# Kernel optimization log

Hardware: AMD Instinct MI355X
Metric: run time of the kernel (lower is better)

Reference implementation:

```python
import jax, jax.numpy as jnp
import numpy as np

NUM_HEADS = 4
NUM_GROUPS = 8
EPS = 1e-5


def setup_inputs() -> dict:
    key = jax.random.key(0)
    ks = jax.random.split(key, 4)
    B, C, H, W = 4, 256, 64, 64
    x = jax.random.normal(ks[0], (B, C, H, W), dtype=jnp.float32)
    gn_w = jnp.ones((C,), dtype=jnp.float32)
    gn_b = jnp.zeros((C,), dtype=jnp.float32)
    # 1x1 convs == per-pixel matmuls; store kernels as [out_ch, in_ch]
    w_qkv = jax.random.normal(ks[1], (3 * C, C), dtype=jnp.float32) * (1.0 / np.sqrt(C))
    b_qkv = jnp.zeros((3 * C,), dtype=jnp.float32)
    w_proj = jax.random.normal(ks[2], (C, C), dtype=jnp.float32) * (1.0 / np.sqrt(C))
    b_proj = jnp.zeros((C,), dtype=jnp.float32)
    return {"x": x, "gn_w": gn_w, "gn_b": gn_b, "w_qkv": w_qkv,
            "b_qkv": b_qkv, "w_proj": w_proj, "b_proj": b_proj}


def reference(x, gn_w, gn_b, w_qkv, b_qkv, w_proj, b_proj):
    B, C, H, W = x.shape
    N = H * W
    nh = NUM_HEADS
    dh = C // nh

    # GroupNorm(8, C)
    xg = x.reshape(B, NUM_GROUPS, C // NUM_GROUPS, N)
    mu = jnp.mean(xg, axis=(2, 3), keepdims=True)
    var = jnp.var(xg, axis=(2, 3), keepdims=True)
    h = ((xg - mu) * jax.lax.rsqrt(var + EPS)).reshape(B, C, N)
    h = h * gn_w[None, :, None] + gn_b[None, :, None]

    # qkv 1x1 conv
    qkv = jnp.einsum('oc,bcn->bon', w_qkv, h) + b_qkv[None, :, None]
    q, k, v = jnp.split(qkv, 3, axis=1)  # each [B, C, N]
    q = q.reshape(B, nh, dh, N)
    k = k.reshape(B, nh, dh, N)
    v = v.reshape(B, nh, dh, N)

    # attn = softmax(q^T k / sqrt(dh)) over last dim -> [B, nh, N, N]
    scores = jnp.einsum('bhdi,bhdj->bhij', q, k) / jnp.sqrt(jnp.array(dh, dtype=x.dtype))
    attn = jax.nn.softmax(scores, axis=-1)

    # out = attn @ v^T, back to channel-major layout
    out = jnp.einsum('bhij,bhdj->bhdi', attn, v).reshape(B, C, N)

    # proj_out 1x1 conv + residual
    out = jnp.einsum('oc,bcn->bon', w_proj, out) + b_proj[None, :, None]
    return x + out.reshape(B, C, H, W)
```

## Files before the change

kernel.cpp:

```cpp
#include <hip/hip_runtime.h>
#include <math.h>

#define N_PIX 4096
#define C_CH  256
#define NH    4
#define DH    64

typedef __attribute__((ext_vector_type(8))) short bf16x8;
typedef __attribute__((ext_vector_type(4))) float f32x4;

static __device__ __forceinline__ unsigned short f2bf(float f) {
  union { float f; unsigned u; } v; v.f = f;
  unsigned r = v.u + 0x7fffu + ((v.u >> 16) & 1u);
  return (unsigned short)(r >> 16);
}
static __device__ __forceinline__ unsigned pk2(float a, float b) {
  return (unsigned)f2bf(a) | ((unsigned)f2bf(b) << 16);
}
static __device__ __forceinline__ unsigned pk2t(float a, float b) {
  return __builtin_amdgcn_perm(__float_as_uint(b), __float_as_uint(a),
                               0x07060302u);
}
#if __has_builtin(__builtin_amdgcn_exp2f)
#define EXP2(x) __builtin_amdgcn_exp2f(x)
#else
#define EXP2(x) exp2f(x)
#endif
static __device__ __forceinline__ int swz(int row, int g) {
  return (row << 6) + ((((row >> 2) ^ row ^ g) & 7) << 3);
}

__global__ __launch_bounds__(256) void gn_part_kernel(
    const float* __restrict__ x, const float* __restrict__ wqkv,
    const float* __restrict__ wproj, float* __restrict__ part,
    unsigned short* __restrict__ wB) {
  const int g = blockIdx.x, b = blockIdx.y, z = blockIdx.z;
  const int t = threadIdx.x;
  {
    const int bid = blockIdx.z * 32 + blockIdx.y * 8 + blockIdx.x;
    const int i = bid * 256 + t;
    const float* src = (i < 49152) ? (wqkv + (size_t)i * 4)
                                   : (wproj + (size_t)(i - 49152) * 4);
    float4 v = *(const float4*)src;
    uint2 u;
    u.x = pk2(v.x, v.y);
    u.y = pk2(v.z, v.w);
    *(uint2*)(wB + (size_t)i * 4) = u;
  }
  const float* base = x + (size_t)(b * C_CH + g * 32 + z * 4) * N_PIX;
  float sum = 0.f, sq = 0.f;
  for (int i = t * 4; i < 4 * N_PIX; i += 256 * 4) {
    float4 v = *(const float4*)(base + i);
    sum += v.x + v.y + v.z + v.w;
    sq  += v.x * v.x + v.y * v.y + v.z * v.z + v.w * v.w;
  }
  for (int off = 32; off >= 1; off >>= 1) {
    sum += __shfl_down(sum, off, 64);
    sq  += __shfl_down(sq,  off, 64);
  }
  __shared__ float ps[4], pq[4];
  if ((t & 63) == 0) { ps[t >> 6] = sum; pq[t >> 6] = sq; }
  __syncthreads();
  if (t == 0) {
    int idx = ((b * 8 + g) * 8 + z) * 2;
    part[idx + 0] = ps[0] + ps[1] + ps[2] + ps[3];
    part[idx + 1] = pq[0] + pq[1] + pq[2] + pq[3];
  }
}

__global__ __launch_bounds__(256) void gn_apply_kernel(
    const float* __restrict__ x, const float* __restrict__ part,
    const float* __restrict__ gn_w, const float* __restrict__ gn_b,
    unsigned short* __restrict__ hT) {
  const int n0 = blockIdx.x * 64;
  const int c0 = blockIdx.y * 64;
  const int b  = blockIdx.z;
  const int t  = threadIdx.x;
  __shared__ unsigned short Ht[64 * 64];
  __shared__ float ls[64], lsh[64];
  if (t < 64) {
    int c = c0 + t;
    int g = c >> 5;
    float S = 0.f, Q = 0.f;
#pragma unroll
    for (int z = 0; z < 8; ++z) {
      int idx = ((b * 8 + g) * 8 + z) * 2;
      S += part[idx + 0];
      Q += part[idx + 1];
    }
    const float inv_cnt = 1.f / (32.f * N_PIX);
    float mu  = S * inv_cnt;
    float var = Q * inv_cnt - mu * mu;
    float rstd = rsqrtf(var + 1e-5f);
    float s = rstd * gn_w[c];
    ls[t]  = s;
    lsh[t] = gn_b[c] - mu * s;
  }
  __syncthreads();
  const int cl = t >> 4;
  const int nl = (t & 15) * 4;
#pragma unroll
  for (int r = 0; r < 4; ++r) {
    int ce = cl + r * 16;
    float sv = ls[ce], sh = lsh[ce];
    float4 v =
        *(const float4*)(x + ((size_t)(b * C_CH + c0 + ce)) * N_PIX + n0 + nl);
#pragma unroll
    for (int i = 0; i < 4; ++i) {
      float f = ((const float*)&v)[i] * sv + sh;
      Ht[swz(nl + i, ce >> 3) + (ce & 7)] = f2bf(f);
    }
  }
  __syncthreads();
  {
    const int row = t >> 2, sg = (t & 3) * 2;
    uint4 o0 = *(const uint4*)&Ht[swz(row, sg + 0)];
    uint4 o1 = *(const uint4*)&Ht[swz(row, sg + 1)];
    size_t go = ((size_t)(b * N_PIX + n0 + row)) * C_CH + c0 + sg * 8;
    *(uint4*)(hT + go) = o0;
    *(uint4*)(hT + go + 8) = o1;
  }
}

__global__ __launch_bounds__(256) void qkv_gemm_kernel(
    const unsigned short* __restrict__ hT, const unsigned short* __restrict__ wB,
    const float* __restrict__ bqkv, unsigned short* __restrict__ qT,
    unsigned short* __restrict__ kT, unsigned short* __restrict__ vO) {
  const int head = blockIdx.x;
  const int n0 = blockIdx.y * 128;
  const int b  = blockIdx.z;
  const int t  = threadIdx.x;
  const int wave = t >> 6, lane = t & 63, quad = lane >> 4, lc = lane & 15;

  __shared__ unsigned short Ws[3 * 64 * 64];
  __shared__ unsigned short Hs[128 * 64];

  f32x4 acc[3][4][2];
#pragma unroll
  for (int ty = 0; ty < 3; ++ty)
#pragma unroll
    for (int i = 0; i < 4; ++i)
#pragma unroll
      for (int j = 0; j < 2; ++j) acc[ty][i][j] = (f32x4){0.f, 0.f, 0.f, 0.f};

  const int wrow = t >> 2, wgb = (t & 3) * 2;
  const int hrow = t >> 1, hgb = (t & 1) * 4;
  const unsigned short* wp =
      wB + (size_t)(head * 64 + wrow) * C_CH + wgb * 8;
  const unsigned short* ap =
      hT + ((size_t)(b * N_PIX + n0 + hrow)) * C_CH + hgb * 8;
  const int wsw0 = swz(wrow, wgb + 0), wsw1 = swz(wrow, wgb + 1);
  int hsw[4];
#pragma unroll
  for (int j = 0; j < 4; ++j) hsw[j] = swz(hrow, hgb + j);

  for (int kc = 0; kc < 4; ++kc) {
    const int k0 = kc * 64;
    __syncthreads();
#pragma unroll
    for (int ty = 0; ty < 3; ++ty) {
      const unsigned short* s0 = wp + (size_t)ty * 256 * C_CH + k0;
      uint4 u0 = *(const uint4*)(s0);
      uint4 u1 = *(const uint4*)(s0 + 8);
      *(uint4*)&Ws[ty * 4096 + wsw0] = u0;
      *(uint4*)&Ws[ty * 4096 + wsw1] = u1;
    }
    {
      const unsigned short* s0 = ap + k0;
#pragma unroll
      for (int j = 0; j < 4; ++j) {
        uint4 u = *(const uint4*)(s0 + j * 8);
        *(uint4*)&Hs[hsw[j]] = u;
      }
    }
    __syncthreads();
#pragma unroll
    for (int kh = 0; kh < 2; ++kh) {
      bf16x8 hf[2];
#pragma unroll
      for (int nt = 0; nt < 2; ++nt)
        hf[nt] = *(const bf16x8*)&Hs[swz(wave * 32 + nt * 16 + lc, kh * 4 + quad)];
#pragma unroll
      for (int ty = 0; ty < 3; ++ty) {
        bf16x8 wf[4];
#pragma unroll
        for (int mt = 0; mt < 4; ++mt)
          wf[mt] =
              *(const bf16x8*)&Ws[ty * 4096 + swz(mt * 16 + lc, kh * 4 + quad)];
        if (ty < 2) {
#pragma unroll
          for (int mt = 0; mt < 4; ++mt)
#pragma unroll
            for (int nt = 0; nt < 2; ++nt)
              acc[ty][mt][nt] = __builtin_amdgcn_mfma_f32_16x16x32_bf16(
                  wf[mt], hf[nt], acc[ty][mt][nt], 0, 0, 0);
        } else {
#pragma unroll
          for (int mt = 0; mt < 4; ++mt)
#pragma unroll
            for (int nt = 0; nt < 2; ++nt)
              acc[2][mt][nt] = __builtin_amdgcn_mfma_f32_16x16x32_bf16(
                  hf[nt], wf[mt], acc[2][mt][nt], 0, 0, 0);
        }
      }
    }
  }

#pragma unroll
  for (int ty = 0; ty < 2; ++ty) {
    unsigned short* dst = (ty == 0) ? qT : kT;
    const float qs = (ty == 0) ? 0.125f * 1.44269504f : 1.0f;
    const int bb = ty * 256 + head * 64;
#pragma unroll
    for (int mt = 0; mt < 4; ++mt)
#pragma unroll
      for (int nt = 0; nt < 2; ++nt) {
        int n = n0 + wave * 32 + nt * 16 + lc;
        int d0 = mt * 16 + quad * 4;
        float b0 = bqkv[bb + d0 + 0], b1 = bqkv[bb + d0 + 1];
        float b2 = bqkv[bb + d0 + 2], b3 = bqkv[bb + d0 + 3];
        uint2 w;
        w.x = pk2((acc[ty][mt][nt][0] + b0) * qs, (acc[ty][mt][nt][1] + b1) * qs);
        w.y = pk2((acc[ty][mt][nt][2] + b2) * qs, (acc[ty][mt][nt][3] + b3) * qs);
        *(uint2*)(dst + ((size_t)((b * NH + head) * N_PIX + n)) * 64 + d0) = w;
      }
  }
  {
    const int bb = 512 + head * 64;
#pragma unroll
    for (int mt = 0; mt < 4; ++mt)
#pragma unroll
      for (int nt = 0; nt < 2; ++nt) {
        int d = mt * 16 + lc;
        float bias = bqkv[bb + d];
        int pix = n0 + wave * 32 + nt * 16 + quad * 4;
        uint2 w;
        w.x = pk2(acc[2][mt][nt][0] + bias, acc[2][mt][nt][1] + bias);
        w.y = pk2(acc[2][mt][nt][2] + bias, acc[2][mt][nt][3] + bias);
        *(uint2*)(vO + ((size_t)((b * NH + head) * 64 + d)) * N_PIX + pix) = w;
      }
  }
}

__global__ __launch_bounds__(256) void attn_kernel(
    const unsigned short* __restrict__ qT, const unsigned short* __restrict__ kT,
    const unsigned short* __restrict__ vO, unsigned short* __restrict__ aT) {
  const int t  = threadIdx.x;
  const int i0 = blockIdx.x * 128;
  const int h  = blockIdx.y;
  const int b  = blockIdx.z;
  const size_t bh = (size_t)(b * NH + h);
  const unsigned short* qp = qT + bh * N_PIX * 64;
  const unsigned short* kp = kT + bh * N_PIX * 64;
  const unsigned short* vp = vO + bh * 64 * N_PIX;

  __shared__ unsigned short Qt[128 * 64];
  __shared__ unsigned short Kt[2 * 64 * 64];
  __shared__ unsigned short Vs[2 * 64 * 64];
  unsigned short* const Ps = Qt;

  const int wave = t >> 6, lane = t & 63, quad = lane >> 4, lc = lane & 15;
  const int qb0 = wave * 32, qb1 = wave * 32 + 16;
  const int srow = t >> 2, sg = (t & 3) * 2;
  const int qrow = t >> 1, qg = (t & 1) * 4;

  {
    const unsigned short* sp = qp + (size_t)(i0 + qrow) * 64 + qg * 8;
#pragma unroll
    for (int i = 0; i < 4; ++i) {
      uint4 u = *(const uint4*)(sp + i * 8);
      *(uint4*)&Qt[swz(qrow, qg + i)] = u;
    }
  }
  __syncthreads();
  bf16x8 aq[2][2];
  aq[0][0] = *(const bf16x8*)&Qt[swz(qb0 + lc, quad)];
  aq[0][1] = *(const bf16x8*)&Qt[swz(qb0 + lc, quad + 4)];
  aq[1][0] = *(const bf16x8*)&Qt[swz(qb1 + lc, quad)];
  aq[1][1] = *(const bf16x8*)&Qt[swz(qb1 + lc, quad + 4)];

  int kof0[4], kof1[4], vof0[4], vof1[4], pw[2][4];
#pragma unroll
  for (int jt = 0; jt < 4; ++jt) {
    kof0[jt] = swz(jt * 16 + lc, quad);
    kof1[jt] = swz(jt * 16 + lc, quad + 4);
    pw[0][jt] = swz(qb0 + lc, jt * 2 + (quad >> 1)) + (quad & 1) * 4;
    pw[1][jt] = swz(qb1 + lc, jt * 2 + (quad >> 1)) + (quad & 1) * 4;
  }
#pragma unroll
  for (int mt = 0; mt < 4; ++mt) {
    vof0[mt] = swz(mt * 16 + lc, quad);
    vof1[mt] = swz(mt * 16 + lc, quad + 4);
  }
  const int pb00 = swz(qb0 + lc, quad), pb01 = swz(qb0 + lc, quad + 4);
  const int pb10 = swz(qb1 + lc, quad), pb11 = swz(qb1 + lc, quad + 4);
  const int sw0 = swz(srow, sg + 0), sw1 = swz(srow, sg + 1);
  const unsigned short* kbase = kp + (size_t)srow * 64 + sg * 8;
  const unsigned short* vbase = vp + (size_t)srow * N_PIX + sg * 8;

  float la0 = 0.f, la1 = 0.f;
  f32x4 od[2][4];
#pragma unroll
  for (int qh = 0; qh < 2; ++qh)
#pragma unroll
    for (int mt = 0; mt < 4; ++mt) od[qh][mt] = (f32x4){0.f, 0.f, 0.f, 0.f};

  {
    uint4 k0 = *(const uint4*)(kbase);
    uint4 k1 = *(const uint4*)(kbase + 8);
    uint4 v0 = *(const uint4*)(vbase);
    uint4 v1 = *(const uint4*)(vbase + 8);
    *(uint4*)&Kt[sw0] = k0;
    *(uint4*)&Kt[sw1] = k1;
    *(uint4*)&Vs[sw0] = v0;
    *(uint4*)&Vs[sw1] = v1;
  }
  __syncthreads();

  {
    uint4 pk0 = *(const uint4*)(kbase + 4096);
    uint4 pk1 = *(const uint4*)(kbase + 4096 + 8);
    uint4 pv0 = *(const uint4*)(vbase + 64);
    uint4 pv1 = *(const uint4*)(vbase + 64 + 8);
#pragma unroll
    for (int jt = 0; jt < 4; ++jt) {
      bf16x8 bk0 = *(const bf16x8*)&Kt[kof0[jt]];
      bf16x8 bk1 = *(const bf16x8*)&Kt[kof1[jt]];
      f32x4 a0 = (f32x4){0.f, 0.f, 0.f, 0.f};
      a0 = __builtin_amdgcn_mfma_f32_16x16x32_bf16(bk0, aq[0][0], a0, 0, 0, 0);
      a0 = __builtin_amdgcn_mfma_f32_16x16x32_bf16(bk1, aq[0][1], a0, 0, 0, 0);
      f32x4 a1 = (f32x4){0.f, 0.f, 0.f, 0.f};
      a1 = __builtin_amdgcn_mfma_f32_16x16x32_bf16(bk0, aq[1][0], a1, 0, 0, 0);
      a1 = __builtin_amdgcn_mfma_f32_16x16x32_bf16(bk1, aq[1][1], a1, 0, 0, 0);
      float e0 = EXP2(a0[0]), e1 = EXP2(a0[1]), e2 = EXP2(a0[2]),
            e3 = EXP2(a0[3]);
      la0 += (e0 + e1) + (e2 + e3);
      uint2 u0;
      u0.x = pk2t(e0, e1);
      u0.y = pk2t(e2, e3);
      *(uint2*)&Ps[pw[0][jt]] = u0;
      float f0 = EXP2(a1[0]), f1 = EXP2(a1[1]), f2 = EXP2(a1[2]),
            f3 = EXP2(a1[3]);
      la1 += (f0 + f1) + (f2 + f3);
      uint2 u1;
      u1.x = pk2t(f0, f1);
      u1.y = pk2t(f2, f3);
      *(uint2*)&Ps[pw[1][jt]] = u1;
    }
    *(uint4*)&Kt[4096 + sw0] = pk0;
    *(uint4*)&Kt[4096 + sw1] = pk1;
    *(uint4*)&Vs[4096 + sw0] = pv0;
    *(uint4*)&Vs[4096 + sw1] = pv1;
  }

  for (int it = 1; it < 64; ++it) {
    const int cb = (it & 1) << 12;
    const int ob = 4096 - cb;
    __syncthreads();
    const size_t kadv = (size_t)((it + 1) & 63) * 4096;
    const size_t vadv = (size_t)((it + 1) & 63) * 64;
    uint4 pk0 = *(const uint4*)(kbase + kadv);
    uint4 pk1 = *(const uint4*)(kbase + kadv + 8);
    uint4 pv0 = *(const uint4*)(vbase + vadv);
    uint4 pv1 = *(const uint4*)(vbase + vadv + 8);

    f32x4 s0[4], s1[4];
#pragma unroll
    for (int jt = 0; jt < 4; ++jt) {
      bf16x8 bk0 = *(const bf16x8*)&Kt[cb + kof0[jt]];
      bf16x8 bk1 = *(const bf16x8*)&Kt[cb + kof1[jt]];
      f32x4 a0 = (f32x4){0.f, 0.f, 0.f, 0.f};
      a0 = __builtin_amdgcn_mfma_f32_16x16x32_bf16(bk0, aq[0][0], a0, 0, 0, 0);
      a0 = __builtin_amdgcn_mfma_f32_16x16x32_bf16(bk1, aq[0][1], a0, 0, 0, 0);
      f32x4 a1 = (f32x4){0.f, 0.f, 0.f, 0.f};
      a1 = __builtin_amdgcn_mfma_f32_16x16x32_bf16(bk0, aq[1][0], a1, 0, 0, 0);
      a1 = __builtin_amdgcn_mfma_f32_16x16x32_bf16(bk1, aq[1][1], a1, 0, 0, 0);
      s0[jt] = a0;
      s1[jt] = a1;
    }

    bf16x8 bp00 = *(const bf16x8*)&Ps[pb00];
    bf16x8 bp01 = *(const bf16x8*)&Ps[pb01];
    bf16x8 bp10 = *(const bf16x8*)&Ps[pb10];
    bf16x8 bp11 = *(const bf16x8*)&Ps[pb11];

#pragma unroll
    for (int mt = 0; mt < 4; ++mt) {
      bf16x8 av0 = *(const bf16x8*)&Vs[ob + vof0[mt]];
      bf16x8 av1 = *(const bf16x8*)&Vs[ob + vof1[mt]];
      od[0][mt] =
          __builtin_amdgcn_mfma_f32_16x16x32_bf16(av0, bp00, od[0][mt], 0, 0, 0);
      od[0][mt] =
          __builtin_amdgcn_mfma_f32_16x16x32_bf16(av1, bp01, od[0][mt], 0, 0, 0);
      od[1][mt] =
          __builtin_amdgcn_mfma_f32_16x16x32_bf16(av0, bp10, od[1][mt], 0, 0, 0);
      od[1][mt] =
          __builtin_amdgcn_mfma_f32_16x16x32_bf16(av1, bp11, od[1][mt], 0, 0, 0);
      float e0 = EXP2(s0[mt][0]), e1 = EXP2(s0[mt][1]), e2 = EXP2(s0[mt][2]),
            e3 = EXP2(s0[mt][3]);
      la0 += (e0 + e1) + (e2 + e3);
      uint2 u0;
      u0.x = pk2t(e0, e1);
      u0.y = pk2t(e2, e3);
      *(uint2*)&Ps[pw[0][mt]] = u0;
      float f0 = EXP2(s1[mt][0]), f1 = EXP2(s1[mt][1]), f2 = EXP2(s1[mt][2]),
            f3 = EXP2(s1[mt][3]);
      la1 += (f0 + f1) + (f2 + f3);
      uint2 u1;
      u1.x = pk2t(f0, f1);
      u1.y = pk2t(f2, f3);
      *(uint2*)&Ps[pw[1][mt]] = u1;
    }

    __syncthreads();
    *(uint4*)&Kt[ob + sw0] = pk0;
    *(uint4*)&Kt[ob + sw1] = pk1;
    *(uint4*)&Vs[ob + sw0] = pv0;
    *(uint4*)&Vs[ob + sw1] = pv1;
  }

  {
    bf16x8 bp00 = *(const bf16x8*)&Ps[pb00];
    bf16x8 bp01 = *(const bf16x8*)&Ps[pb01];
    bf16x8 bp10 = *(const bf16x8*)&Ps[pb10];
    bf16x8 bp11 = *(const bf16x8*)&Ps[pb11];
#pragma unroll
    for (int mt = 0; mt < 4; ++mt) {
      bf16x8 av0 = *(const bf16x8*)&Vs[4096 + vof0[mt]];
      bf16x8 av1 = *(const bf16x8*)&Vs[4096 + vof1[mt]];
      od[0][mt] =
          __builtin_amdgcn_mfma_f32_16x16x32_bf16(av0, bp00, od[0][mt], 0, 0, 0);
      od[0][mt] =
          __builtin_amdgcn_mfma_f32_16x16x32_bf16(av1, bp01, od[0][mt], 0, 0, 0);
      od[1][mt] =
          __builtin_amdgcn_mfma_f32_16x16x32_bf16(av0, bp10, od[1][mt], 0, 0, 0);
      od[1][mt] =
          __builtin_amdgcn_mfma_f32_16x16x32_bf16(av1, bp11, od[1][mt], 0, 0, 0);
    }
  }

  la0 += __shfl_xor(la0, 16, 64);
  la0 += __shfl_xor(la0, 32, 64);
  la1 += __shfl_xor(la1, 16, 64);
  la1 += __shfl_xor(la1, 32, 64);
  float inv0 = 1.f / la0;
  float inv1 = 1.f / la1;

#pragma unroll
  for (int mt = 0; mt < 4; ++mt) {
    uint2 u0, u1;
    u0.x = pk2(od[0][mt][0] * inv0, od[0][mt][1] * inv0);
    u0.y = pk2(od[0][mt][2] * inv0, od[0][mt][3] * inv0);
    u1.x = pk2(od[1][mt][0] * inv1, od[1][mt][1] * inv1);
    u1.y = pk2(od[1][mt][2] * inv1, od[1][mt][3] * inv1);
    *(uint2*)&Ps[swz(qb0 + lc, mt * 2 + (quad >> 1)) + (quad & 1) * 4] = u0;
    *(uint2*)&Ps[swz(qb1 + lc, mt * 2 + (quad >> 1)) + (quad & 1) * 4] = u1;
  }
  __syncthreads();
  {
    size_t go = ((size_t)(b * N_PIX + i0 + qrow)) * C_CH + h * 64 + qg * 8;
#pragma unroll
    for (int i = 0; i < 4; ++i) {
      uint4 o = *(const uint4*)&Ps[swz(qrow, qg + i)];
      *(uint4*)(aT + go + i * 8) = o;
    }
  }
}

__global__ __launch_bounds__(256) void proj_gemm_kernel(
    const unsigned short* __restrict__ aT, const unsigned short* __restrict__ wPB,
    const float* __restrict__ bproj, const float* __restrict__ x,
    float* __restrict__ out) {
  const int m0 = blockIdx.x * 64;
  const int n0 = blockIdx.y * 128;
  const int b  = blockIdx.z;
  const int t  = threadIdx.x;
  const int wave = t >> 6, lane = t & 63, quad = lane >> 4, lc = lane & 15;

  __shared__ unsigned short Ws[64 * 64];
  __shared__ unsigned short Hs[128 * 64];

  f32x4 acc[4][2];
#pragma unroll
  for (int i = 0; i < 4; ++i)
#pragma unroll
    for (int j = 0; j < 2; ++j) acc[i][j] = (f32x4){0.f, 0.f, 0.f, 0.f};

  const int wrow = t >> 2, wgb = (t & 3) * 2;
  const int hrow = t >> 1, hgb = (t & 1) * 4;
  const unsigned short* wp = wPB + (size_t)(m0 + wrow) * C_CH;
  const unsigned short* ap =
      aT + ((size_t)(b * N_PIX + n0 + hrow)) * C_CH + hgb * 8;

  for (int k0 = 0; k0 < C_CH; k0 += 64) {
    __syncthreads();
    {
      const unsigned short* s0 = wp + k0 + wgb * 8;
      uint4 u0 = *(const uint4*)(s0);
      uint4 u1 = *(const uint4*)(s0 + 8);
      *(uint4*)&Ws[swz(wrow, wgb + 0)] = u0;
      *(uint4*)&Ws[swz(wrow, wgb + 1)] = u1;
    }
    {
      const unsigned short* s0 = ap + k0;
#pragma unroll
      for (int j = 0; j < 4; ++j) {
        uint4 u = *(const uint4*)(s0 + j * 8);
        *(uint4*)&Hs[swz(hrow, hgb + j)] = u;
      }
    }
    __syncthreads();
#pragma unroll
    for (int kh = 0; kh < 2; ++kh) {
      bf16x8 wf[4], hf[2];
#pragma unroll
      for (int mt = 0; mt < 4; ++mt)
        wf[mt] = *(const bf16x8*)&Ws[swz(mt * 16 + lc, kh * 4 + quad)];
#pragma unroll
      for (int nt = 0; nt < 2; ++nt)
        hf[nt] = *(const bf16x8*)&Hs[swz(wave * 32 + nt * 16 + lc, kh * 4 + quad)];
#pragma unroll
      for (int mt = 0; mt < 4; ++mt)
#pragma unroll
        for (int nt = 0; nt < 2; ++nt)
          acc[mt][nt] = __builtin_amdgcn_mfma_f32_16x16x32_bf16(
              wf[mt], hf[nt], acc[mt][nt], 0, 0, 0);
    }
  }
#pragma unroll
  for (int mt = 0; mt < 4; ++mt) {
#pragma unroll
    for (int nt = 0; nt < 2; ++nt) {
      int n = n0 + wave * 32 + nt * 16 + lc;
#pragma unroll
      for (int r = 0; r < 4; ++r) {
        int c = m0 + mt * 16 + quad * 4 + r;
        size_t gi = ((size_t)(b * C_CH + c)) * N_PIX + n;
        out[gi] = acc[mt][nt][r] + bproj[c] + x[gi];
      }
    }
  }
}

extern "C" void kernel_launch(void* const* d_in, const int* in_sizes, int n_in,
                              void* d_out, int out_size, void* d_ws,
                              size_t ws_size, hipStream_t stream) {
  const float* x      = (const float*)d_in[0];
  const float* gn_w   = (const float*)d_in[1];
  const float* gn_b   = (const float*)d_in[2];
  const float* w_qkv  = (const float*)d_in[3];
  const float* b_qkv  = (const float*)d_in[4];
  const float* w_proj = (const float*)d_in[5];
  const float* b_proj = (const float*)d_in[6];
  float* out = (float*)d_out;

  float* ws   = (float*)d_ws;
  float* part = ws + 2048;
  unsigned short* qT = (unsigned short*)(ws + 4096);
  unsigned short* kT = qT + (size_t)4194304;
  unsigned short* vO = kT + (size_t)4194304;
  unsigned short* aT = vO + (size_t)4194304;
  unsigned short* hT = aT + (size_t)4194304;
  unsigned short* wB = hT + (size_t)4194304;
  unsigned short* wPB = wB + (size_t)49152 * 4;

  gn_part_kernel<<<dim3(8, 4, 8), dim3(256), 0, stream>>>(x, w_qkv, w_proj,
                                                          part, wB);
  gn_apply_kernel<<<dim3(64, 4, 4), dim3(256), 0, stream>>>(x, part, gn_w,
                                                            gn_b, hT);
  qkv_gemm_kernel<<<dim3(4, 32, 4), dim3(256), 0, stream>>>(
      hT, wB, b_qkv, qT, kT, vO);
  attn_kernel<<<dim3(32, 4, 4), dim3(256), 0, stream>>>(qT, kT, vO, aT);
  proj_gemm_kernel<<<dim3(4, 32, 4), dim3(256), 0, stream>>>(
      aT, wPB, b_proj, x, out);
}
```

Measured before the change: 209.9 us.

## Process 128-key tiles per iteration with register prefetch in attention loop

Restructures the attention main loop to load 128 keys/values per iteration (two 64-wide halves) into shared memory instead of double-buffered 64-key tiles. This halves the number of loop iterations and barrier pairs, while prefetching the next tile into registers. Each iteration does QK for both halves and PV across them within one tile, which raises register pressure and removes the cross-iteration overlap of global loads with the old double buffer.

```diff
diff --git a/kernel.cpp b/kernel.cpp
--- a/kernel.cpp
+++ b/kernel.cpp
@@ -255,14 +255,23 @@
   const unsigned short* vp = vO + bh * 64 * N_PIX;
 
   __shared__ unsigned short Qt[128 * 64];
-  __shared__ unsigned short Kt[2 * 64 * 64];
+  __shared__ unsigned short Kt[128 * 64];
   __shared__ unsigned short Vs[2 * 64 * 64];
   unsigned short* const Ps = Qt;
 
   const int wave = t >> 6, lane = t & 63, quad = lane >> 4, lc = lane & 15;
   const int qb0 = wave * 32, qb1 = wave * 32 + 16;
-  const int srow = t >> 2, sg = (t & 3) * 2;
   const int qrow = t >> 1, qg = (t & 1) * 4;
+
+  const int kr = t >> 1, kgb = (t & 1) * 4;
+  const int vr = t >> 2, vgb = (t & 3) * 2;
+  int ksw[4], vsw[2];
+#pragma unroll
+  for (int i = 0; i < 4; ++i) ksw[i] = swz(kr, kgb + i);
+#pragma unroll
+  for (int i = 0; i < 2; ++i) vsw[i] = swz(vr, vgb + i);
+  const unsigned short* kbase = kp + (size_t)kr * 64 + kgb * 8;
+  const unsigned short* vbase = vp + (size_t)vr * N_PIX + vgb * 8;
 
   {
     const unsigned short* sp = qp + (size_t)(i0 + qrow) * 64 + qg * 8;
@@ -272,6 +281,14 @@
       *(uint4*)&Qt[swz(qrow, qg + i)] = u;
     }
   }
+  uint4 pk[4], pv[2][2];
+#pragma unroll
+  for (int i = 0; i < 4; ++i) pk[i] = *(const uint4*)(kbase + i * 8);
+#pragma unroll
+  for (int hh = 0; hh < 2; ++hh)
+#pragma unroll
+    for (int i = 0; i < 2; ++i)
+      pv[hh][i] = *(const uint4*)(vbase + hh * 64 + i * 8);
   __syncthreads();
   bf16x8 aq[2][2];
   aq[0][0] = *(const bf16x8*)&Qt[swz(qb0 + lc, quad)];
@@ -279,11 +296,14 @@
   aq[1][0] = *(const bf16x8*)&Qt[swz(qb1 + lc, quad)];
   aq[1][1] = *(const bf16x8*)&Qt[swz(qb1 + lc, quad + 4)];
 
-  int kof0[4], kof1[4], vof0[4], vof1[4], pw[2][4];
+  int kof0[2][4], kof1[2][4], vof0[4], vof1[4], pw[2][4];
 #pragma unroll
   for (int jt = 0; jt < 4; ++jt) {
-    kof0[jt] = swz(jt * 16 + lc, quad);
-    kof1[jt] = swz(jt * 16 + lc, quad + 4);
+#pragma unroll
+    for (int hh = 0; hh < 2; ++hh) {
+      kof0[hh][jt] = swz(hh * 64 + jt * 16 + lc, quad);
+      kof1[hh][jt] = swz(hh * 64 + jt * 16 + lc, quad + 4);
+    }
     pw[0][jt] = swz(qb0 + lc, jt * 2 + (quad >> 1)) + (quad & 1) * 4;
     pw[1][jt] = swz(qb1 + lc, jt * 2 + (quad >> 1)) + (quad & 1) * 4;
   }
@@ -294,9 +314,6 @@
   }
   const int pb00 = swz(qb0 + lc, quad), pb01 = swz(qb0 + lc, quad + 4);
   const int pb10 = swz(qb1 + lc, quad), pb11 = swz(qb1 + lc, quad + 4);
-  const int sw0 = swz(srow, sg + 0), sw1 = swz(srow, sg + 1);
-  const unsigned short* kbase = kp + (size_t)srow * 64 + sg * 8;
-  const unsigned short* vbase = vp + (size_t)srow * N_PIX + sg * 8;
 
   float la0 = 0.f, la1 = 0.f;
   f32x4 od[2][4];
@@ -305,27 +322,26 @@
 #pragma unroll
     for (int mt = 0; mt < 4; ++mt) od[qh][mt] = (f32x4){0.f, 0.f, 0.f, 0.f};
 
-  {
-    uint4 k0 = *(const uint4*)(kbase);
-    uint4 k1 = *(const uint4*)(kbase + 8);
-    uint4 v0 = *(const uint4*)(vbase);
-    uint4 v1 = *(const uint4*)(vbase + 8);
-    *(uint4*)&Kt[sw0] = k0;
-    *(uint4*)&Kt[sw1] = k1;
-    *(uint4*)&Vs[sw0] = v0;
-    *(uint4*)&Vs[sw1] = v1;
-  }
+#pragma unroll
+  for (int i = 0; i < 4; ++i) *(uint4*)&Kt[ksw[i]] = pk[i];
+#pragma unroll
+  for (int hh = 0; hh < 2; ++hh)
+#pragma unroll
+    for (int i = 0; i < 2; ++i) *(uint4*)&Vs[hh * 4096 + vsw[i]] = pv[hh][i];
   __syncthreads();
-
-  {
-    uint4 pk0 = *(const uint4*)(kbase + 4096);
-    uint4 pk1 = *(const uint4*)(kbase + 4096 + 8);
-    uint4 pv0 = *(const uint4*)(vbase + 64);
-    uint4 pv1 = *(const uint4*)(vbase + 64 + 8);
+#pragma unroll
+  for (int i = 0; i < 4; ++i) pk[i] = *(const uint4*)(kbase + 8192 + i * 8);
+#pragma unroll
+  for (int hh = 0; hh < 2; ++hh)
+#pragma unroll
+    for (int i = 0; i < 2; ++i)
+      pv[hh][i] = *(const uint4*)(vbase + 128 + hh * 64 + i * 8);
+
+  for (int it = 0; it < 32; ++it) {
 #pragma unroll
     for (int jt = 0; jt < 4; ++jt) {
-      bf16x8 bk0 = *(const bf16x8*)&Kt[kof0[jt]];
-      bf16x8 bk1 = *(const bf16x8*)&Kt[kof1[jt]];
+      bf16x8 bk0 = *(const bf16x8*)&Kt[kof0[0][jt]];
+      bf16x8 bk1 = *(const bf16x8*)&Kt[kof1[0][jt]];
       f32x4 a0 = (f32x4){0.f, 0.f, 0.f, 0.f};
       a0 = __builtin_amdgcn_mfma_f32_16x16x32_bf16(bk0, aq[0][0], a0, 0, 0, 0);
       a0 = __builtin_amdgcn_mfma_f32_16x16x32_bf16(bk1, aq[0][1], a0, 0, 0, 0);
@@ -347,28 +363,16 @@
       u1.y = pk2t(f2, f3);
       *(uint2*)&Ps[pw[1][jt]] = u1;
     }
-    *(uint4*)&Kt[4096 + sw0] = pk0;
-    *(uint4*)&Kt[4096 + sw1] = pk1;
-    *(uint4*)&Vs[4096 + sw0] = pv0;
-    *(uint4*)&Vs[4096 + sw1] = pv1;
-  }
-
-  for (int it = 1; it < 64; ++it) {
-    const int cb = (it & 1) << 12;
-    const int ob = 4096 - cb;
-    __syncthreads();
-    const size_t kadv = (size_t)((it + 1) & 63) * 4096;
-    const size_t vadv = (size_t)((it + 1) & 63) * 64;
-    uint4 pk0 = *(const uint4*)(kbase + kadv);
-    uint4 pk1 = *(const uint4*)(kbase + kadv + 8);
-    uint4 pv0 = *(const uint4*)(vbase + vadv);
-    uint4 pv1 = *(const uint4*)(vbase + vadv + 8);
-
+
+    bf16x8 bp00 = *(const bf16x8*)&Ps[pb00];
+    bf16x8 bp01 = *(const bf16x8*)&Ps[pb01];
+    bf16x8 bp10 = *(const bf16x8*)&Ps[pb10];
+    bf16x8 bp11 = *(const bf16x8*)&Ps[pb11];
     f32x4 s0[4], s1[4];
 #pragma unroll
     for (int jt = 0; jt < 4; ++jt) {
-      bf16x8 bk0 = *(const bf16x8*)&Kt[cb + kof0[jt]];
-      bf16x8 bk1 = *(const bf16x8*)&Kt[cb + kof1[jt]];
+      bf16x8 bk0 = *(const bf16x8*)&Kt[kof0[1][jt]];
+      bf16x8 bk1 = *(const bf16x8*)&Kt[kof1[1][jt]];
       f32x4 a0 = (f32x4){0.f, 0.f, 0.f, 0.f};
       a0 = __builtin_amdgcn_mfma_f32_16x16x32_bf16(bk0, aq[0][0], a0, 0, 0, 0);
       a0 = __builtin_amdgcn_mfma_f32_16x16x32_bf16(bk1, aq[0][1], a0, 0, 0, 0);
@@ -378,16 +382,10 @@
       s0[jt] = a0;
       s1[jt] = a1;
     }
-
-    bf16x8 bp00 = *(const bf16x8*)&Ps[pb00];
-    bf16x8 bp01 = *(const bf16x8*)&Ps[pb01];
-    bf16x8 bp10 = *(const bf16x8*)&Ps[pb10];
-    bf16x8 bp11 = *(const bf16x8*)&Ps[pb11];
-
 #pragma unroll
     for (int mt = 0; mt < 4; ++mt) {
-      bf16x8 av0 = *(const bf16x8*)&Vs[ob + vof0[mt]];
-      bf16x8 av1 = *(const bf16x8*)&Vs[ob + vof1[mt]];
+      bf16x8 av0 = *(const bf16x8*)&Vs[vof0[mt]];
+      bf16x8 av1 = *(const bf16x8*)&Vs[vof1[mt]];
       od[0][mt] =
           __builtin_amdgcn_mfma_f32_16x16x32_bf16(av0, bp00, od[0][mt], 0, 0, 0);
       od[0][mt] =
@@ -412,31 +410,42 @@
       *(uint2*)&Ps[pw[1][mt]] = u1;
     }
 
-    __syncthreads();
-    *(uint4*)&Kt[ob + sw0] = pk0;
-    *(uint4*)&Kt[ob + sw1] = pk1;
-    *(uint4*)&Vs[ob + sw0] = pv0;
-    *(uint4*)&Vs[ob + sw1] = pv1;
-  }
-
-  {
-    bf16x8 bp00 = *(const bf16x8*)&Ps[pb00];
-    bf16x8 bp01 = *(const bf16x8*)&Ps[pb01];
-    bf16x8 bp10 = *(const bf16x8*)&Ps[pb10];
-    bf16x8 bp11 = *(const bf16x8*)&Ps[pb11];
+    bf16x8 cp00 = *(const bf16x8*)&Ps[pb00];
+    bf16x8 cp01 = *(const bf16x8*)&Ps[pb01];
+    bf16x8 cp10 = *(const bf16x8*)&Ps[pb10];
+    bf16x8 cp11 = *(const bf16x8*)&Ps[pb11];
 #pragma unroll
     for (int mt = 0; mt < 4; ++mt) {
       bf16x8 av0 = *(const bf16x8*)&Vs[4096 + vof0[mt]];
       bf16x8 av1 = *(const bf16x8*)&Vs[4096 + vof1[mt]];
       od[0][mt] =
-          __builtin_amdgcn_mfma_f32_16x16x32_bf16(av0, bp00, od[0][mt], 0, 0, 0);
+          __builtin_amdgcn_mfma_f32_16x16x32_bf16(av0, cp00, od[0][mt], 0, 0, 0);
       od[0][mt] =
-          __builtin_amdgcn_mfma_f32_16x16x32_bf16(av1, bp01, od[0][mt], 0, 0, 0);
+          __builtin_amdgcn_mfma_f32_16x16x32_bf16(av1, cp01, od[0][mt], 0, 0, 0);
       od[1][mt] =
-          __builtin_amdgcn_mfma_f32_16x16x32_bf16(av0, bp10, od[1][mt], 0, 0, 0);
+          __builtin_amdgcn_mfma_f32_16x16x32_bf16(av0, cp10, od[1][mt], 0, 0, 0);
       od[1][mt] =
-          __builtin_amdgcn_mfma_f32_16x16x32_bf16(av1, bp11, od[1][mt], 0, 0, 0);
-    }
+          __builtin_amdgcn_mfma_f32_16x16x32_bf16(av1, cp11, od[1][mt], 0, 0, 0);
+    }
+
+    __syncthreads();
+#pragma unroll
+    for (int i = 0; i < 4; ++i) *(uint4*)&Kt[ksw[i]] = pk[i];
+#pragma unroll
+    for (int hh = 0; hh < 2; ++hh)
+#pragma unroll
+      for (int i = 0; i < 2; ++i) *(uint4*)&Vs[hh * 4096 + vsw[i]] = pv[hh][i];
+    __syncthreads();
+    const size_t kadv = (size_t)(((it + 2) & 31) * 128) * 64;
+    const size_t vadv = (size_t)(((it + 2) & 31) * 128);
+#pragma unroll
+    for (int i = 0; i < 4; ++i)
+      pk[i] = *(const uint4*)(kbase + kadv + i * 8);
+#pragma unroll
+    for (int hh = 0; hh < 2; ++hh)
+#pragma unroll
+      for (int i = 0; i < 2; ++i)
+        pv[hh][i] = *(const uint4*)(vbase + vadv + hh * 64 + i * 8);
   }
 
   la0 += __shfl_xor(la0, 16, 64);
```

Result: slower. 297.7 us (+41.9%).
